# Optimization experiments

Measured on AMD Instinct MI355X. Metric: run time of the kernel, lower is better.

## Reference

```python
import jax, jax.numpy as jnp
import numpy as np

B, IN, OUT, G = 64, 8192, 8192, 64
NG = IN // G  # groups per row


def setup_inputs() -> dict:
    key = jax.random.key(0)
    k1, k2, k3, k4 = jax.random.split(key, 4)
    x = jax.random.normal(k1, (B, IN), dtype=jnp.float32)
    # packed 2-bit codes: 4 codes per byte, LSB-first (matches _pack2)
    w_packed = jax.random.randint(k2, (OUT, IN // 4), 0, 256, dtype=jnp.int32).astype(jnp.uint8)
    # scales from _calc_group_qparams are positive (max_abs/1.5); zp is always 2
    scales = jax.random.uniform(k3, (OUT, NG), dtype=jnp.float32, minval=0.01, maxval=0.1)
    zps = jnp.full((OUT, NG), 2, dtype=jnp.int32)
    bias = jax.random.normal(k4, (OUT,), dtype=jnp.float32) * 0.01
    return {"x": x, "w_packed": w_packed, "scales": scales, "zps": zps, "bias": bias}


def _dequant(w_packed, scales, zps):
    # unpack: byte -> 4 two-bit codes, LSB first (matches _unpack2)
    out_f = w_packed.shape[0]
    codes = jnp.stack([(w_packed >> s) & 3 for s in (0, 2, 4, 6)], axis=-1)  # [OUT, IN//4, 4]
    q = codes.reshape(out_f, NG, G).astype(jnp.int32)                        # [OUT, NG, G]
    # per-group dequant: (q - zp) * scale
    w = (q - zps[:, :, None]).astype(jnp.float32) * scales[:, :, None]
    return w.reshape(out_f, IN)                                              # [OUT, IN]


def reference(x, w_packed, scales, zps, bias):
    w = _dequant(w_packed, scales, zps)  # [OUT, IN] fp32
    # original accumulates xg @ wg.T per group; equivalent to full x @ w.T
    return x @ w.T + bias                # [B, OUT]
```

## Files before the change

kernel.cpp:

```cpp
#include <hip/hip_runtime.h>
#include <hip/hip_bf16.h>

#define B_    64
#define IN_   8192
#define OUT_  8192
#define NG_   128
#define PB_   2048
#define KSPLIT 16
#define KC    512

typedef float    f32x16 __attribute__((ext_vector_type(16)));
typedef short    s16x8  __attribute__((ext_vector_type(8)));
typedef _Float16 f16x4  __attribute__((ext_vector_type(4)));

#define OFF_WQ   (1u << 20)
#define OFF_SQ   (17u << 20)
#define OFF_ZF   (19u << 20)
#define OFF_PART (20u << 20)

__global__ __launch_bounds__(256) void k_prep(
    const float* __restrict__ x, const unsigned char* __restrict__ wp,
    const float* __restrict__ scales, const int* __restrict__ zps,
    uint4* __restrict__ xfrag, unsigned char* __restrict__ wq,
    uint4* __restrict__ sq, int* __restrict__ zflags)
{
    __shared__ int zf;
    const int bid = blockIdx.x, tid = threadIdx.x;

    if (bid < 512) {
        const int c = tid & 15, r = tid >> 4;
        const unsigned v = ((const unsigned*)wp)[tid];
        const bool u8mode = __any((int)(v > 255u));
        uint4 buf[8];
        if (u8mode) {
            const uint4* src = (const uint4*)(wp + (bid * 16 + r) * PB_ + c * 128);
#pragma unroll
            for (int u = 0; u < 8; ++u) buf[u] = src[u];
        } else {
            const int* src = (const int*)wp + (bid * 16 + r) * PB_ + c * 128;
#pragma unroll
            for (int u = 0; u < 8; ++u) {
                unsigned d[4];
#pragma unroll
                for (int w = 0; w < 4; ++w) {
                    const int* p = src + u * 16 + w * 4;
                    d[w] = (unsigned)(p[0] & 0xFF) | ((unsigned)(p[1] & 0xFF) << 8) |
                           ((unsigned)(p[2] & 0xFF) << 16) | ((unsigned)(p[3] & 0xFF) << 24);
                }
                buf[u] = (uint4){d[0], d[1], d[2], d[3]};
            }
        }
        uint4* dst = (uint4*)(wq + ((unsigned)c * OUT_ + bid * 16 + r) * 128);
#pragma unroll
        for (int u = 0; u < 8; ++u) dst[u] = buf[u];
    } else if (bid < 576) {
        const int b2 = bid - 512;
        const int kidx = b2 >> 2, prt = b2 & 3;
#pragma unroll
        for (int i = 0; i < 4; ++i) {
            const int idx = prt * 1024 + i * 256 + tid;
            const int sg = idx >> 6, lane = idx & 63;
            const int t = sg >> 1, mt = sg & 1;
            const int h = lane >> 5, m = lane & 31;
            const float* src = x + (mt * 32 + m) * IN_ + kidx * KC + h * 256 + t * 8;
            const float4 f0 = *(const float4*)src;
            const float4 f1 = *(const float4*)(src + 4);
            __hip_bfloat162 h0 = __float22bfloat162_rn(make_float2(f0.x, f0.y));
            __hip_bfloat162 h1 = __float22bfloat162_rn(make_float2(f0.z, f0.w));
            __hip_bfloat162 h2 = __float22bfloat162_rn(make_float2(f1.x, f1.y));
            __hip_bfloat162 h3 = __float22bfloat162_rn(make_float2(f1.z, f1.w));
            uint4 o;
            o.x = *(unsigned*)&h0; o.y = *(unsigned*)&h1;
            o.z = *(unsigned*)&h2; o.w = *(unsigned*)&h3;
            xfrag[kidx * 4096 + idx] = o;
        }
    } else {
        const int b3 = bid - 576;
        if (tid < 128) {
            const int n = b3 * 128 + tid;
#pragma unroll
            for (int kidx = 0; kidx < 16; ++kidx) {
                const float* sp = scales + n * NG_ + kidx * 8;
                const float4 s0 = *(const float4*)sp;
                const float4 s1 = *(const float4*)(sp + 4);
                __hip_bfloat162 h0 = __float22bfloat162_rn(make_float2(s0.x, s0.y));
                __hip_bfloat162 h1 = __float22bfloat162_rn(make_float2(s0.z, s0.w));
                __hip_bfloat162 h2 = __float22bfloat162_rn(make_float2(s1.x, s1.y));
                __hip_bfloat162 h3 = __float22bfloat162_rn(make_float2(s1.z, s1.w));
                uint4 o;
                o.x = *(unsigned*)&h0; o.y = *(unsigned*)&h1;
                o.z = *(unsigned*)&h2; o.w = *(unsigned*)&h3;
                sq[(unsigned)kidx * OUT_ + n] = o;
            }
        }
        if (tid == 0) zf = 0;
        __syncthreads();
        int bad = 0;
        const int4* zp4 = (const int4*)zps + b3 * 4096;
#pragma unroll
        for (int i = 0; i < 16; ++i) {
            const int4 z = zp4[i * 256 + tid];
            bad |= (z.x != 2) | (z.y != 2) | (z.z != 2) | (z.w != 2);
        }
        if (bad) zf = 1;
        __syncthreads();
        if (tid == 0) zflags[b3] = zf;
    }
}

__global__ __launch_bounds__(256, 2) void k_main(
    const uint4* __restrict__ xfrag, const unsigned char* __restrict__ wq,
    const uint2* __restrict__ sq2, const int* __restrict__ zflags,
    const int* __restrict__ zps, _Float16* __restrict__ part)
{
    __shared__ uint4 x_lds[4096];

    const int tid = threadIdx.x, wave = tid >> 6, lane = tid & 63;
    const int h = lane >> 5, n32 = lane & 31;
    const int kidx = blockIdx.x & (KSPLIT - 1);
    const int nblk = blockIdx.x >> 4;
    const int colbase = nblk * 256 + wave * 64;

    int ncol[2];
    uint2 sv[2];
#pragma unroll
    for (int cg = 0; cg < 2; ++cg) {
        ncol[cg] = colbase + cg * 32 + n32;
        sv[cg] = sq2[((unsigned)kidx * OUT_ + ncol[cg]) * 2 + h];
    }
    const int zv = zflags[lane];

#pragma unroll
    for (int i = 0; i < 16; ++i) {
        const int sg = wave * 16 + i;
        const uint4* src = xfrag + kidx * 4096 + sg * 64 + lane;
        __builtin_amdgcn_global_load_lds(
            (const __attribute__((address_space(1))) unsigned*)src,
            (__attribute__((address_space(3))) unsigned*)((char*)x_lds + sg * 1024),
            16, 0, 0);
    }
    const bool zgen = __any(zv != 0);
    __syncthreads();
    __builtin_amdgcn_sched_barrier(0);

    unsigned tl[2][4], th[2][4];
#pragma unroll
    for (int cg = 0; cg < 2; ++cg) {
#pragma unroll
        for (int gg = 0; gg < 4; ++gg) {
            const unsigned dwv = (gg >> 1) ? sv[cg].y : sv[cg].x;
            const unsigned s16 = (gg & 1) ? (dwv >> 16) : (dwv & 0xFFFFu);
            if (!zgen) {
                const unsigned m1 = s16 | 0x8000u;
                const unsigned m2 = (s16 + 0x0080u) | 0x8000u;
                tl[cg][gg] = m2 | (m1 << 16);
                th[cg][gg] = s16 << 16;
            } else {
                union { unsigned u; float f; } sf; sf.u = s16 << 16;
                const int g = kidx * 8 + h * 4 + gg;
                const float zf = (float)zps[ncol[cg] * NG_ + g];
                const float v0 = (0.f - zf) * sf.f, v1 = (1.f - zf) * sf.f;
                const float v2 = (2.f - zf) * sf.f, v3 = (3.f - zf) * sf.f;
                __hip_bfloat162 lo = __float22bfloat162_rn(make_float2(v0, v1));
                __hip_bfloat162 hi = __float22bfloat162_rn(make_float2(v2, v3));
                tl[cg][gg] = *(unsigned*)&lo;
                th[cg][gg] = *(unsigned*)&hi;
            }
        }
    }

    f32x16 acc[2][2];
#pragma unroll
    for (int cg = 0; cg < 2; ++cg)
#pragma unroll
        for (int mt = 0; mt < 2; ++mt)
#pragma unroll
            for (int r = 0; r < 16; ++r) acc[cg][mt][r] = 0.f;

    const uint4* wb0 = (const uint4*)(wq + ((unsigned)kidx * OUT_ + ncol[0]) * 128 + h * 64);
    const uint4* wb1 = (const uint4*)(wq + ((unsigned)kidx * OUT_ + ncol[1]) * 128 + h * 64);
    uint4 wcur0 = wb0[0], wcur1 = wb1[0];
#pragma unroll
    for (int c = 0; c < 4; ++c) {
        uint4 wn0, wn1;
        if (c < 3) { wn0 = wb0[c + 1]; wn1 = wb1[c + 1]; }
#pragma unroll
        for (int dw = 0; dw < 4; ++dw) {
#pragma unroll
            for (int hf = 0; hf < 2; ++hf) {
                const int t = c * 8 + dw * 2 + hf;
                union { uint4 u4; s16x8 s8; } av[2];
#pragma unroll
                for (int mt = 0; mt < 2; ++mt)
                    av[mt].u4 = x_lds[(t * 2 + mt) * 64 + lane];
#pragma unroll
                for (int cg = 0; cg < 2; ++cg) {
                    const uint4 wc = cg ? wcur1 : wcur0;
                    const unsigned wdw = ((const unsigned*)&wc)[dw];
                    const unsigned u = hf ? (wdw >> 16) : (wdw & 0xFFFFu);
                    const unsigned tlv = tl[cg][c], thv = th[cg][c];
                    union { unsigned w_[4]; s16x8 s8; } bf;
#pragma unroll
                    for (int m = 0; m < 4; ++m) {
                        const unsigned c0 = (u >> (4 * m)) & 3u;
                        const unsigned c1 = (u >> (4 * m + 2)) & 3u;
                        const unsigned sel = 0x01000100u + c0 * 0x0202u + c1 * 0x02020000u;
                        bf.w_[m] = __builtin_amdgcn_perm(thv, tlv, sel);
                    }
#pragma unroll
                    for (int mt = 0; mt < 2; ++mt)
                        acc[cg][mt] = __builtin_amdgcn_mfma_f32_32x32x16_bf16(
                            av[mt].s8, bf.s8, acc[cg][mt], 0, 0, 0);
                }
            }
        }
        if (c < 3) { wcur0 = wn0; wcur1 = wn1; }
    }

    _Float16* pp = part + kidx * (B_ * OUT_);
#pragma unroll
    for (int cg = 0; cg < 2; ++cg) {
        const int col = ncol[cg];
#pragma unroll
        for (int mt = 0; mt < 2; ++mt)
#pragma unroll
            for (int r = 0; r < 16; ++r) {
                const int row = (r & 3) + 8 * (r >> 2) + 4 * h;
                pp[(mt * 32 + row) * OUT_ + col] = (_Float16)acc[cg][mt][r];
            }
    }
}

__global__ __launch_bounds__(256) void k_reduce(const _Float16* __restrict__ part,
                                                const float* __restrict__ bias,
                                                float* __restrict__ out) {
    const int gtid = blockIdx.x * 256 + threadIdx.x;
    const int b  = gtid >> 11;
    const int n0 = (gtid & 2047) * 4;
    float4 s = *(const float4*)(bias + n0);
#pragma unroll
    for (int p = 0; p < KSPLIT; ++p) {
        const f16x4 v = *(const f16x4*)(part + p * (B_ * OUT_) + b * OUT_ + n0);
        s.x += (float)v[0]; s.y += (float)v[1];
        s.z += (float)v[2]; s.w += (float)v[3];
    }
    *(float4*)(out + b * OUT_ + n0) = s;
}

extern "C" void kernel_launch(void* const* d_in, const int* in_sizes, int n_in,
                              void* d_out, int out_size, void* d_ws, size_t ws_size,
                              hipStream_t stream) {
    const float*         x      = (const float*)d_in[0];
    const unsigned char* wp     = (const unsigned char*)d_in[1];
    const float*         scales = (const float*)d_in[2];
    const int*           zps    = (const int*)d_in[3];
    const float*         bias   = (const float*)d_in[4];
    float*               out    = (float*)d_out;

    char* ws = (char*)d_ws;
    uint4*         xfrag = (uint4*)ws;
    unsigned char* wq    = (unsigned char*)(ws + OFF_WQ);
    uint4*         sq    = (uint4*)(ws + OFF_SQ);
    int*           zfl   = (int*)(ws + OFF_ZF);
    _Float16*      part  = (_Float16*)(ws + OFF_PART);

    k_prep<<<640, 256, 0, stream>>>(x, wp, scales, zps, xfrag, wq, sq, zfl);
    k_main<<<512, 256, 0, stream>>>(xfrag, wq, (const uint2*)sq, zfl, zps, part);
    k_reduce<<<512, 256, 0, stream>>>(part, bias, out);
}
```

Baseline: 137.6 us.

## Fuse prep, main GEMM and reduce into one persistent kernel with grid barriers

Replaces the three-kernel pipeline with a single persistent kernel of 512 blocks that prepares x fragments, scales and zero-point flags, syncs on a global atomic barrier, runs the MFMA split-K GEMM, then syncs again and performs the split-K reduction with bias. In u8 mode weights are read directly from the packed input in their original layout, which drops the transposed weight copy, and the weight loads are issued before the prep work so they overlap it. The aim is to remove kernel launch gaps and the extra weight-copy traffic. In exchange it relies on all 512 blocks being co-resident for the spin barriers, which risks deadlock, and adds atomic and sleep overhead.

```diff
diff --git a/kernel.cpp b/kernel.cpp
--- a/kernel.cpp
+++ b/kernel.cpp
@@ -8,127 +8,147 @@
 #define PB_   2048
 #define KSPLIT 16
 #define KC    512
+#define NBLK  512
 
 typedef float    f32x16 __attribute__((ext_vector_type(16)));
 typedef short    s16x8  __attribute__((ext_vector_type(8)));
 typedef _Float16 f16x4  __attribute__((ext_vector_type(4)));
 
-#define OFF_WQ   (1u << 20)
-#define OFF_SQ   (17u << 20)
-#define OFF_ZF   (19u << 20)
-#define OFF_PART (20u << 20)
-
-__global__ __launch_bounds__(256) void k_prep(
+#define OFF_SQ   (1u << 20)
+#define OFF_PART (4u << 20)
+#define OFF_WQ8  (20u << 20)
+#define OFF_CTL  (40u << 20)
+
+__global__ __launch_bounds__(64) void k_init(int* ctl) {
+    if (threadIdx.x < 4) ctl[threadIdx.x] = 0;
+}
+
+__device__ __forceinline__ void gbar(int* cnt, int tid) {
+    __syncthreads();
+    if (tid == 0) {
+        __threadfence();
+        atomicAdd(cnt, 1);
+        while (__hip_atomic_load(cnt, __ATOMIC_ACQUIRE,
+                                 __HIP_MEMORY_SCOPE_AGENT) < NBLK)
+            __builtin_amdgcn_s_sleep(8);
+        __threadfence();
+    }
+    __syncthreads();
+}
+
+__global__ __launch_bounds__(256, 2) void k_fused(
     const float* __restrict__ x, const unsigned char* __restrict__ wp,
     const float* __restrict__ scales, const int* __restrict__ zps,
-    uint4* __restrict__ xfrag, unsigned char* __restrict__ wq,
-    uint4* __restrict__ sq, int* __restrict__ zflags)
+    const float* __restrict__ bias, float* __restrict__ out, char* __restrict__ ws)
 {
-    __shared__ int zf;
-    const int bid = blockIdx.x, tid = threadIdx.x;
-
-    if (bid < 512) {
-        const int c = tid & 15, r = tid >> 4;
-        const unsigned v = ((const unsigned*)wp)[tid];
-        const bool u8mode = __any((int)(v > 255u));
-        uint4 buf[8];
-        if (u8mode) {
-            const uint4* src = (const uint4*)(wp + (bid * 16 + r) * PB_ + c * 128);
-#pragma unroll
-            for (int u = 0; u < 8; ++u) buf[u] = src[u];
-        } else {
-            const int* src = (const int*)wp + (bid * 16 + r) * PB_ + c * 128;
-#pragma unroll
-            for (int u = 0; u < 8; ++u) {
-                unsigned d[4];
-#pragma unroll
-                for (int w = 0; w < 4; ++w) {
-                    const int* p = src + u * 16 + w * 4;
-                    d[w] = (unsigned)(p[0] & 0xFF) | ((unsigned)(p[1] & 0xFF) << 8) |
-                           ((unsigned)(p[2] & 0xFF) << 16) | ((unsigned)(p[3] & 0xFF) << 24);
-                }
-                buf[u] = (uint4){d[0], d[1], d[2], d[3]};
-            }
-        }
-        uint4* dst = (uint4*)(wq + ((unsigned)c * OUT_ + bid * 16 + r) * 128);
-#pragma unroll
-        for (int u = 0; u < 8; ++u) dst[u] = buf[u];
-    } else if (bid < 576) {
-        const int b2 = bid - 512;
-        const int kidx = b2 >> 2, prt = b2 & 3;
-#pragma unroll
-        for (int i = 0; i < 4; ++i) {
-            const int idx = prt * 1024 + i * 256 + tid;
-            const int sg = idx >> 6, lane = idx & 63;
-            const int t = sg >> 1, mt = sg & 1;
-            const int h = lane >> 5, m = lane & 31;
-            const float* src = x + (mt * 32 + m) * IN_ + kidx * KC + h * 256 + t * 8;
-            const float4 f0 = *(const float4*)src;
-            const float4 f1 = *(const float4*)(src + 4);
-            __hip_bfloat162 h0 = __float22bfloat162_rn(make_float2(f0.x, f0.y));
-            __hip_bfloat162 h1 = __float22bfloat162_rn(make_float2(f0.z, f0.w));
-            __hip_bfloat162 h2 = __float22bfloat162_rn(make_float2(f1.x, f1.y));
-            __hip_bfloat162 h3 = __float22bfloat162_rn(make_float2(f1.z, f1.w));
+    __shared__ uint4 x_lds[4096];
+
+    uint4*         xfrag = (uint4*)ws;
+    uint4*         sq    = (uint4*)(ws + OFF_SQ);
+    _Float16*      part  = (_Float16*)(ws + OFF_PART);
+    unsigned char* wq8   = (unsigned char*)(ws + OFF_WQ8);
+    int*           ctl   = (int*)(ws + OFF_CTL);
+
+    const int tid = threadIdx.x, bid = blockIdx.x;
+    const int wave = tid >> 6, lane = tid & 63;
+    const int h = lane >> 5, n32 = lane & 31;
+    const int kidx = bid & (KSPLIT - 1), nblk = bid >> 4;
+    const int colbase = nblk * 256 + wave * 64;
+    int ncol[2];
+    ncol[0] = colbase + n32;
+    ncol[1] = colbase + 32 + n32;
+
+    const unsigned wv = ((const unsigned*)wp)[tid];
+    const bool u8m = __any((int)(wv > 255u));
+
+    uint4 w[2][4];
+    if (u8m) {
+#pragma unroll
+        for (int cg = 0; cg < 2; ++cg) {
+            const uint4* wb = (const uint4*)(wp + (unsigned)ncol[cg] * PB_ + kidx * 128 + h * 64);
+#pragma unroll
+            for (int c = 0; c < 4; ++c) w[cg][c] = wb[c];
+        }
+    }
+
+    if (bid < 256) {
+        const int idx = bid * 256 + tid;
+        const int kx = idx >> 12, slot = idx & 4095;
+        const int sg = slot >> 6, ln = slot & 63;
+        const int t = sg >> 1, mt = sg & 1;
+        const int hh = ln >> 5, m = ln & 31;
+        const float* src = x + (mt * 32 + m) * IN_ + kx * KC + hh * 256 + t * 8;
+        const float4 f0 = *(const float4*)src;
+        const float4 f1 = *(const float4*)(src + 4);
+        __hip_bfloat162 h0 = __float22bfloat162_rn(make_float2(f0.x, f0.y));
+        __hip_bfloat162 h1 = __float22bfloat162_rn(make_float2(f0.z, f0.w));
+        __hip_bfloat162 h2 = __float22bfloat162_rn(make_float2(f1.x, f1.y));
+        __hip_bfloat162 h3 = __float22bfloat162_rn(make_float2(f1.z, f1.w));
+        uint4 o;
+        o.x = *(unsigned*)&h0; o.y = *(unsigned*)&h1;
+        o.z = *(unsigned*)&h2; o.w = *(unsigned*)&h3;
+        xfrag[idx] = o;
+    } else {
+#pragma unroll
+        for (int r = 0; r < 2; ++r) {
+            const int e = (bid - 256) * 512 + r * 256 + tid;
+            const int n = e >> 4, kx = e & 15;
+            const float* sp = scales + n * NG_ + kx * 8;
+            const float4 s0 = *(const float4*)sp;
+            const float4 s1 = *(const float4*)(sp + 4);
+            __hip_bfloat162 h0 = __float22bfloat162_rn(make_float2(s0.x, s0.y));
+            __hip_bfloat162 h1 = __float22bfloat162_rn(make_float2(s0.z, s0.w));
+            __hip_bfloat162 h2 = __float22bfloat162_rn(make_float2(s1.x, s1.y));
+            __hip_bfloat162 h3 = __float22bfloat162_rn(make_float2(s1.z, s1.w));
             uint4 o;
             o.x = *(unsigned*)&h0; o.y = *(unsigned*)&h1;
             o.z = *(unsigned*)&h2; o.w = *(unsigned*)&h3;
-            xfrag[kidx * 4096 + idx] = o;
-        }
-    } else {
-        const int b3 = bid - 576;
-        if (tid < 128) {
-            const int n = b3 * 128 + tid;
-#pragma unroll
-            for (int kidx = 0; kidx < 16; ++kidx) {
-                const float* sp = scales + n * NG_ + kidx * 8;
-                const float4 s0 = *(const float4*)sp;
-                const float4 s1 = *(const float4*)(sp + 4);
-                __hip_bfloat162 h0 = __float22bfloat162_rn(make_float2(s0.x, s0.y));
-                __hip_bfloat162 h1 = __float22bfloat162_rn(make_float2(s0.z, s0.w));
-                __hip_bfloat162 h2 = __float22bfloat162_rn(make_float2(s1.x, s1.y));
-                __hip_bfloat162 h3 = __float22bfloat162_rn(make_float2(s1.z, s1.w));
-                uint4 o;
-                o.x = *(unsigned*)&h0; o.y = *(unsigned*)&h1;
-                o.z = *(unsigned*)&h2; o.w = *(unsigned*)&h3;
-                sq[(unsigned)kidx * OUT_ + n] = o;
-            }
-        }
-        if (tid == 0) zf = 0;
-        __syncthreads();
+            sq[(unsigned)kx * OUT_ + n] = o;
+        }
+    }
+    {
         int bad = 0;
-        const int4* zp4 = (const int4*)zps + b3 * 4096;
-#pragma unroll
-        for (int i = 0; i < 16; ++i) {
+        const int4* zp4 = (const int4*)zps + bid * 512;
+#pragma unroll
+        for (int i = 0; i < 2; ++i) {
             const int4 z = zp4[i * 256 + tid];
             bad |= (z.x != 2) | (z.y != 2) | (z.z != 2) | (z.w != 2);
         }
-        if (bad) zf = 1;
-        __syncthreads();
-        if (tid == 0) zflags[b3] = zf;
-    }
-}
-
-__global__ __launch_bounds__(256, 2) void k_main(
-    const uint4* __restrict__ xfrag, const unsigned char* __restrict__ wq,
-    const uint2* __restrict__ sq2, const int* __restrict__ zflags,
-    const int* __restrict__ zps, _Float16* __restrict__ part)
-{
-    __shared__ uint4 x_lds[4096];
-
-    const int tid = threadIdx.x, wave = tid >> 6, lane = tid & 63;
-    const int h = lane >> 5, n32 = lane & 31;
-    const int kidx = blockIdx.x & (KSPLIT - 1);
-    const int nblk = blockIdx.x >> 4;
-    const int colbase = nblk * 256 + wave * 64;
-
-    int ncol[2];
+        if (__any(bad) && lane == 0) atomicOr(&ctl[2], 1);
+    }
+    if (!u8m) {
+        const int* src = (const int*)wp + bid * 32768;
+        uint4* dst = (uint4*)(wq8 + bid * 32768);
+#pragma unroll
+        for (int i = 0; i < 8; ++i) {
+            const int j = tid + i * 256;
+            const int* p = src + j * 16;
+            unsigned d[4];
+#pragma unroll
+            for (int ww = 0; ww < 4; ++ww)
+                d[ww] = (unsigned)(p[ww*4] & 0xFF) | ((unsigned)(p[ww*4+1] & 0xFF) << 8) |
+                        ((unsigned)(p[ww*4+2] & 0xFF) << 16) | ((unsigned)(p[ww*4+3] & 0xFF) << 24);
+            dst[j] = (uint4){d[0], d[1], d[2], d[3]};
+        }
+    }
+
+    gbar(&ctl[0], tid);
+
+    if (!u8m) {
+#pragma unroll
+        for (int cg = 0; cg < 2; ++cg) {
+            const uint4* wb = (const uint4*)(wq8 + (unsigned)ncol[cg] * PB_ + kidx * 128 + h * 64);
+#pragma unroll
+            for (int c = 0; c < 4; ++c) w[cg][c] = wb[c];
+        }
+    }
     uint2 sv[2];
-#pragma unroll
-    for (int cg = 0; cg < 2; ++cg) {
-        ncol[cg] = colbase + cg * 32 + n32;
+    const uint2* sq2 = (const uint2*)sq;
+#pragma unroll
+    for (int cg = 0; cg < 2; ++cg)
         sv[cg] = sq2[((unsigned)kidx * OUT_ + ncol[cg]) * 2 + h];
-    }
-    const int zv = zflags[lane];
+    const bool zgen =
+        (__hip_atomic_load(&ctl[2], __ATOMIC_RELAXED, __HIP_MEMORY_SCOPE_AGENT) != 0);
 
 #pragma unroll
     for (int i = 0; i < 16; ++i) {
@@ -139,9 +159,7 @@
             (__attribute__((address_space(3))) unsigned*)((char*)x_lds + sg * 1024),
             16, 0, 0);
     }
-    const bool zgen = __any(zv != 0);
     __syncthreads();
-    __builtin_amdgcn_sched_barrier(0);
 
     unsigned tl[2][4], th[2][4];
 #pragma unroll
@@ -177,13 +195,8 @@
 #pragma unroll
             for (int r = 0; r < 16; ++r) acc[cg][mt][r] = 0.f;
 
-    const uint4* wb0 = (const uint4*)(wq + ((unsigned)kidx * OUT_ + ncol[0]) * 128 + h * 64);
-    const uint4* wb1 = (const uint4*)(wq + ((unsigned)kidx * OUT_ + ncol[1]) * 128 + h * 64);
-    uint4 wcur0 = wb0[0], wcur1 = wb1[0];
 #pragma unroll
     for (int c = 0; c < 4; ++c) {
-        uint4 wn0, wn1;
-        if (c < 3) { wn0 = wb0[c + 1]; wn1 = wb1[c + 1]; }
 #pragma unroll
         for (int dw = 0; dw < 4; ++dw) {
 #pragma unroll
@@ -195,8 +208,7 @@
                     av[mt].u4 = x_lds[(t * 2 + mt) * 64 + lane];
 #pragma unroll
                 for (int cg = 0; cg < 2; ++cg) {
-                    const uint4 wc = cg ? wcur1 : wcur0;
-                    const unsigned wdw = ((const unsigned*)&wc)[dw];
+                    const unsigned wdw = ((const unsigned*)&w[cg][c])[dw];
                     const unsigned u = hf ? (wdw >> 16) : (wdw & 0xFFFFu);
                     const unsigned tlv = tl[cg][c], thv = th[cg][c];
                     union { unsigned w_[4]; s16x8 s8; } bf;
@@ -214,29 +226,24 @@
                 }
             }
         }
-        if (c < 3) { wcur0 = wn0; wcur1 = wn1; }
     }
 
     _Float16* pp = part + kidx * (B_ * OUT_);
 #pragma unroll
     for (int cg = 0; cg < 2; ++cg) {
-        const int col = ncol[cg];
 #pragma unroll
         for (int mt = 0; mt < 2; ++mt)
 #pragma unroll
             for (int r = 0; r < 16; ++r) {
                 const int row = (r & 3) + 8 * (r >> 2) + 4 * h;
-                pp[(mt * 32 + row) * OUT_ + col] = (_Float16)acc[cg][mt][r];
+                pp[(mt * 32 + row) * OUT_ + ncol[cg]] = (_Float16)acc[cg][mt][r];
             }
     }
-}
-
-__global__ __launch_bounds__(256) void k_reduce(const _Float16* __restrict__ part,
-                                                const float* __restrict__ bias,
-                                                float* __restrict__ out) {
-    const int gtid = blockIdx.x * 256 + threadIdx.x;
-    const int b  = gtid >> 11;
-    const int n0 = (gtid & 2047) * 4;
+
+    gbar(&ctl[1], tid);
+
+    const int i4 = (bid * 256 + tid) * 4;
+    const int b = i4 >> 13, n0 = i4 & (OUT_ - 1);
     float4 s = *(const float4*)(bias + n0);
 #pragma unroll
     for (int p = 0; p < KSPLIT; ++p) {
@@ -244,7 +251,7 @@
         s.x += (float)v[0]; s.y += (float)v[1];
         s.z += (float)v[2]; s.w += (float)v[3];
     }
-    *(float4*)(out + b * OUT_ + n0) = s;
+    *(float4*)(out + i4) = s;
 }
 
 extern "C" void kernel_launch(void* const* d_in, const int* in_sizes, int n_in,
@@ -256,15 +263,8 @@
     const int*           zps    = (const int*)d_in[3];
     const float*         bias   = (const float*)d_in[4];
     float*               out    = (float*)d_out;
-
-    char* ws = (char*)d_ws;
-    uint4*         xfrag = (uint4*)ws;
-    unsigned char* wq    = (unsigned char*)(ws + OFF_WQ);
-    uint4*         sq    = (uint4*)(ws + OFF_SQ);
-    int*           zfl   = (int*)(ws + OFF_ZF);
-    _Float16*      part  = (_Float16*)(ws + OFF_PART);
-
-    k_prep<<<640, 256, 0, stream>>>(x, wp, scales, zps, xfrag, wq, sq, zfl);
-    k_main<<<512, 256, 0, stream>>>(xfrag, wq, (const uint2*)sq, zfl, zps, part);
-    k_reduce<<<512, 256, 0, stream>>>(part, bias, out);
-}
+    int*                 ctl    = (int*)((char*)d_ws + OFF_CTL);
+
+    k_init<<<1, 64, 0, stream>>>(ctl);
+    k_fused<<<NBLK, 256, 0, stream>>>(x, wp, scales, zps, bias, out, (char*)d_ws);
+}
```

New measurement: 277.1 us. 2.01x slower.
